# Kernel optimization log

Hardware: AMD Instinct MI355X
Metric: run time of the kernel (lower is better)

## Reference

```python
import jax, jax.numpy as jnp
import numpy as np

B, N, E0, F_IN, H, EMB, VEC, DPI = 1024, 256, 2048, 6, 32, 32, 26, 512


def setup_inputs() -> dict:
    key = jax.random.key(0)
    ks = jax.random.split(key, 16)
    # fixed urban scene graph, shared by every batch element, with self-loops
    src0 = jax.random.randint(ks[0], (E0,), 0, N, dtype=jnp.int32)
    dst0 = jax.random.randint(ks[1], (E0,), 0, N, dtype=jnp.int32)
    loops = jnp.arange(N, dtype=jnp.int32)
    src = jnp.concatenate([src0, loops])
    dst = jnp.concatenate([dst0, loops])

    s = 0.05
    return {
        "graph_feats": jax.random.normal(ks[2], (B, N, F_IN), jnp.float32),
        "vector": jax.random.normal(ks[3], (B, VEC), jnp.float32),
        "src": src,
        "dst": dst,
        "W1": jax.random.normal(ks[4], (F_IN, H), jnp.float32) * s,
        "b1": jnp.zeros((H,), jnp.float32),
        "W2": jax.random.normal(ks[5], (H, H), jnp.float32) * s,
        "b2": jnp.zeros((H,), jnp.float32),
        "W3": jax.random.normal(ks[6], (H, H), jnp.float32) * s,
        "b3": jnp.zeros((H,), jnp.float32),
        "W_emb": jax.random.normal(ks[7], (H, EMB), jnp.float32) * s,
        "b_emb": jnp.zeros((EMB,), jnp.float32),
        "W_pi": jax.random.normal(ks[8], (VEC + EMB, DPI), jnp.float32) * s,
        "b_pi": jnp.zeros((DPI,), jnp.float32),
        "W_vf": jax.random.normal(ks[9], (VEC + EMB, DPI), jnp.float32) * s,
        "b_vf": jnp.zeros((DPI,), jnp.float32),
    }


def _edge_norm(src, dst, n_nodes):
    # DGL GraphConv norm='both': out_deg(src)^-1/2 * in_deg(dst)^-1/2
    ones = jnp.ones(src.shape[0], jnp.float32)
    deg_out = jax.ops.segment_sum(ones, src, num_segments=n_nodes)
    deg_in = jax.ops.segment_sum(ones, dst, num_segments=n_nodes)
    inv_o = jnp.where(deg_out > 0, deg_out ** -0.5, 0.0)
    inv_i = jnp.where(deg_in > 0, deg_in ** -0.5, 0.0)
    return inv_o[src] * inv_i[dst]  # [E]


def _gconv(h, src, dst, norm, W, b):
    # h: [B, N, F]; symmetric-normalized aggregation then linear (DGL GraphConv)
    msg = h[:, src, :] * norm[None, :, None]          # [B, E, F]
    agg = jnp.zeros_like(h).at[:, dst, :].add(msg)     # [B, N, F]
    return agg @ W + b


def reference(graph_feats, vector, src, dst, W1, b1, W2, b2, W3, b3,
              W_emb, b_emb, W_pi, b_pi, W_vf, b_vf):
    n_nodes = graph_feats.shape[1]
    norm = _edge_norm(src, dst, n_nodes)
    h = jax.nn.relu(_gconv(graph_feats, src, dst, norm, W1, b1))
    h = jax.nn.relu(_gconv(h, src, dst, norm, W2, b2))
    h = jax.nn.relu(_gconv(h, src, dst, norm, W3, b3))  # three_layers=True
    hg = jnp.mean(h, axis=1)                 # dgl.mean_nodes -> [B, H]
    emb = hg @ W_emb + b_emb                 # [B, EMB]
    comb = jnp.concatenate([vector[:, :26], emb], axis=1)  # [B, 58]
    pi = jax.nn.relu(comb @ W_pi + b_pi)
    vf = jax.nn.relu(comb @ W_vf + b_vf)
    return pi, vf
```

## Files before the change

### kernel.cpp

```cpp
#include <hip/hip_runtime.h>
#include <hip/hip_fp16.h>

#define B_    1024
#define N_    256
#define E_    2304
#define EPT_  9
#define FIN_  6
#define VEC_  26
#define HSTR_ 40
#define BPB_  2

typedef _Float16 half8 __attribute__((ext_vector_type(8)));
typedef float    f32x4 __attribute__((ext_vector_type(4)));

__global__ __launch_bounds__(512) void fused_kernel(
    const float* __restrict__ gf,
    const float* __restrict__ vec,
    const int* __restrict__ src, const int* __restrict__ dst,
    const float* __restrict__ W1, const float* __restrict__ b1,
    const float* __restrict__ W2, const float* __restrict__ b2,
    const float* __restrict__ W3, const float* __restrict__ b3,
    const float* __restrict__ We, const float* __restrict__ be,
    const float* __restrict__ Wpi, const float* __restrict__ bpi,
    const float* __restrict__ Wvf, const float* __restrict__ bvf,
    float2* __restrict__ out)
{
    __shared__ __align__(16) __half hbuf[BPB_][N_ * HSTR_];
    __shared__ unsigned int packedE[E_];
    __shared__ float part[BPB_][8 * 33];
    __shared__ float hgl[BPB_][32];
    __shared__ float combS[BPB_][64];
    __shared__ int   wsum[4];

    const int t  = threadIdx.x;
    const int u  = t & 255;
    const int bh = t >> 8;
    const int b0 = blockIdx.x * BPB_;
    const int lane = t & 63, wv = t >> 6;

    int*   deg_o  = (int*)&hbuf[0][0];
    int*   deg_i  = (int*)&hbuf[0][0] + 256;
    int*   scanA  = (int*)&hbuf[0][0] + 512;
    int*   cursor = (int*)&hbuf[0][0] + 768;
    int*   perm   = (int*)&hbuf[0][0] + 1024;
    float* inv_o  = (float*)&hbuf[0][0] + 1280;
    float* inv_i  = (float*)&hbuf[0][0] + 1536;
    int*   bcnt   = (int*)&hbuf[0][0] + 1792;
    int*   boff   = (int*)&hbuf[0][0] + 1856;

    if (t < 256) {
        deg_o[t] = 0; deg_i[t] = 0;
        if (t < 64) bcnt[t] = 0;
    }
    __syncthreads();

    int sB[EPT_], dB[EPT_];
    if (t < 256) {
#pragma unroll
        for (int i = 0; i < EPT_; ++i) { int e = t + 256 * i; sB[i] = src[e]; dB[i] = dst[e]; }
#pragma unroll
        for (int i = 0; i < EPT_; ++i) { atomicAdd(&deg_o[sB[i]], 1); atomicAdd(&deg_i[dB[i]], 1); }
    }
    __syncthreads();

    int x = 0, dI = 0, bucket = 0;
    if (t < 256) {
        dI = deg_i[t];
        {
            int dO = deg_o[t];
            inv_o[t] = dO > 0 ? rsqrtf((float)dO) : 0.f;
            inv_i[t] = dI > 0 ? rsqrtf((float)dI) : 0.f;
        }
        x = dI;
#pragma unroll
        for (int d = 1; d < 64; d <<= 1) {
            int y = __shfl_up(x, d, 64);
            if (lane >= d) x += y;
        }
        if (lane == 63) wsum[wv] = x;
        bucket = dI > 63 ? 63 : dI;
        atomicAdd(&bcnt[bucket], 1);
    }
    __syncthreads();

    if (t < 256) {
        int prefix = 0;
#pragma unroll
        for (int w = 0; w < 3; ++w) if (w < wv) prefix += wsum[w];
        int incl = x + prefix;
        scanA[t]  = incl;
        cursor[t] = incl - dI;
    }
    if (t < 64) {
        int c = bcnt[t], xx = c;
#pragma unroll
        for (int d = 1; d < 64; d <<= 1) {
            int y = __shfl_up(xx, d, 64);
            if (lane >= d) xx += y;
        }
        boff[t] = xx - c;
    }
    __syncthreads();

    if (t < 256) {
        { int pos = atomicAdd(&boff[bucket], 1); perm[pos] = t; }
#pragma unroll
        for (int i = 0; i < EPT_; ++i) {
            int s = sB[i], dd = dB[i];
            int pos = atomicAdd(&cursor[dd], 1);
            float nrm = inv_o[s] * inv_i[dd];
            unsigned short hh = __half_as_ushort(__float2half(nrm));
            packedE[pos] = ((unsigned int)s << 16) | (unsigned int)hh;
        }
    }
    __syncthreads();

    const int node = perm[u];
    const int end  = scanA[node];
    const int beg  = end - deg_i[node];
    __syncthreads();

    {
        const float* g = gf + (size_t)(b0 + bh) * (N_ * FIN_);
        for (int i = u; i < N_ * 8; i += 256) {
            int n = i >> 3, k = i & 7;
            hbuf[bh][n * HSTR_ + k] = __float2half((k < FIN_) ? g[n * FIN_ + k] : 0.f);
        }
    }
    __syncthreads();

    const __half2 z2 = __float2half2_rn(0.f);

    {
        __half2 a2[4] = {z2, z2, z2, z2};
        for (int e = beg; e < end; ++e) {
            unsigned int uu = packedE[e];
            __half2 w2 = __half2half2(__ushort_as_half((unsigned short)(uu & 0xffffu)));
            int ro = (uu >> 16) * HSTR_;
            union { float4 f4; __half2 h2[4]; } r;
            r.f4 = *(const float4*)&hbuf[bh][ro];
#pragma unroll
            for (int q = 0; q < 4; ++q) a2[q] = __hfma2(w2, r.h2[q], a2[q]);
        }
        float o[32];
#pragma unroll
        for (int j = 0; j < 32; ++j) o[j] = b1[j];
#pragma unroll
        for (int k = 0; k < FIN_; ++k) {
            float ak = (k & 1) ? __high2float(a2[k >> 1]) : __low2float(a2[k >> 1]);
            const float* wr = &W1[k * 32];
#pragma unroll
            for (int j = 0; j < 32; ++j) o[j] += ak * wr[j];
        }
        __syncthreads();
        union { float4 f4; __half2 h2[4]; } w;
        float4* row = (float4*)&hbuf[bh][node * HSTR_];
#pragma unroll
        for (int q = 0; q < 4; ++q) {
#pragma unroll
            for (int r = 0; r < 4; ++r)
                w.h2[r] = __floats2half2_rn(fmaxf(o[8*q + 2*r], 0.f), fmaxf(o[8*q + 2*r + 1], 0.f));
            row[q] = w.f4;
        }
    }
    __syncthreads();

    const int m16  = lane & 15;
    const int q4   = lane >> 4;
    const int slab = (wv & 3) * 64;
    const int wb   = wv >> 2;

    for (int L = 0; L < 2; ++L) {
        const float* Wl = (L == 0) ? W2 : W3;
        const float* Bl = (L == 0) ? b2 : b3;

        half8 bfrag[2];
        float bias_c[2];
#pragma unroll
        for (int cb = 0; cb < 2; ++cb) {
            int col = m16 + 16 * cb;
#pragma unroll
            for (int j = 0; j < 8; ++j)
                bfrag[cb][j] = (_Float16)Wl[(q4 * 8 + j) * 32 + col];
            bias_c[cb] = Bl[col];
        }

        __half2 acc2[16];
#pragma unroll
        for (int j = 0; j < 16; ++j) acc2[j] = z2;
        for (int e = beg; e < end; ++e) {
            unsigned int uu = packedE[e];
            __half2 w2 = __half2half2(__ushort_as_half((unsigned short)(uu & 0xffffu)));
            int ro = (uu >> 16) * HSTR_;
            const float4* hr = (const float4*)&hbuf[bh][ro];
            union { float4 f4; __half2 h2[4]; } r0, r1, r2, r3;
            r0.f4 = hr[0]; r1.f4 = hr[1]; r2.f4 = hr[2]; r3.f4 = hr[3];
#pragma unroll
            for (int q = 0; q < 4; ++q) {
                acc2[q]      = __hfma2(w2, r0.h2[q], acc2[q]);
                acc2[4 + q]  = __hfma2(w2, r1.h2[q], acc2[4 + q]);
                acc2[8 + q]  = __hfma2(w2, r2.h2[q], acc2[8 + q]);
                acc2[12 + q] = __hfma2(w2, r3.h2[q], acc2[12 + q]);
            }
        }
        __syncthreads();
        {
            union { float4 f4; __half2 h2[4]; } w;
            float4* row = (float4*)&hbuf[bh][node * HSTR_];
#pragma unroll
            for (int q = 0; q < 4; ++q) {
#pragma unroll
                for (int r = 0; r < 4; ++r) w.h2[r] = acc2[4 * q + r];
                row[q] = w.f4;
            }
        }
        __syncthreads();

        {
            half8 afrag[4];
#pragma unroll
            for (int g = 0; g < 4; ++g) {
                union { float4 f4; half8 h8; } uf;
                uf.f4 = *(const float4*)&hbuf[wb][(slab + g * 16 + m16) * HSTR_ + q4 * 8];
                afrag[g] = uf.h8;
            }
            f32x4 D[4][2];
#pragma unroll
            for (int g = 0; g < 4; ++g) {
#pragma unroll
                for (int cb = 0; cb < 2; ++cb) {
                    f32x4 c = {bias_c[cb], bias_c[cb], bias_c[cb], bias_c[cb]};
                    D[g][cb] = __builtin_amdgcn_mfma_f32_16x16x32_f16(afrag[g], bfrag[cb], c, 0, 0, 0);
                }
            }
#pragma unroll
            for (int g = 0; g < 4; ++g) {
#pragma unroll
                for (int cb = 0; cb < 2; ++cb) {
#pragma unroll
                    for (int r = 0; r < 4; ++r) {
                        float v = fmaxf(D[g][cb][r], 0.f);
                        hbuf[wb][(slab + g * 16 + q4 * 4 + r) * HSTR_ + cb * 16 + m16] = __float2half(v);
                    }
                }
            }
        }
        __syncthreads();
    }

    {
        int j = u & 31, g8 = u >> 5;
        float s = 0.f;
        for (int i = 0; i < 32; ++i)
            s += __half2float(hbuf[bh][(g8 * 32 + i) * HSTR_ + j]);
        part[bh][g8 * 33 + j] = s;
    }
    __syncthreads();
    if (t < 64) {
        int bb = t >> 5, j = t & 31;
        float sum = 0.f;
#pragma unroll
        for (int g8 = 0; g8 < 8; ++g8) sum += part[bb][g8 * 33 + j];
        hgl[bb][j] = sum * (1.0f / 256.0f);
    }
    if (t < BPB_ * VEC_) {
        int bb = t / VEC_, j = t - bb * VEC_;
        combS[bb][j] = vec[(b0 + bb) * VEC_ + j];
    }
    __syncthreads();

    if (t < 64) {
        int bb = t >> 5, j = t & 31;
        float v = be[j];
#pragma unroll
        for (int k = 0; k < 32; ++k) v += hgl[bb][k] * We[k * 32 + j];
        combS[bb][VEC_ + j] = v;
    }
    __syncthreads();

    {
        const float* Wm = (bh == 0) ? Wpi : Wvf;
        const float* bm = (bh == 0) ? bpi : bvf;
        const float2 bp = ((const float2*)bm)[u];
        float2 a0 = bp, a1 = bp;
        const float2* Wr = (const float2*)Wm;
        for (int k = 0; k < VEC_ + 32; ++k) {
            float2 a = Wr[k * 256 + u];
            float c0 = combS[0][k];
            float c1 = combS[1][k];
            a0.x += c0 * a.x; a0.y += c0 * a.y;
            a1.x += c1 * a.x; a1.y += c1 * a.y;
        }
        int base = bh * 262144;
        out[base + b0 * 256 + u]       = make_float2(fmaxf(a0.x, 0.f), fmaxf(a0.y, 0.f));
        out[base + (b0 + 1) * 256 + u] = make_float2(fmaxf(a1.x, 0.f), fmaxf(a1.y, 0.f));
    }
}

extern "C" void kernel_launch(void* const* d_in, const int* in_sizes, int n_in,
                              void* d_out, int out_size, void* d_ws, size_t ws_size,
                              hipStream_t stream)
{
    fused_kernel<<<B_ / BPB_, 512, 0, stream>>>(
        (const float*)d_in[0], (const float*)d_in[1],
        (const int*)d_in[2], (const int*)d_in[3],
        (const float*)d_in[4], (const float*)d_in[5],
        (const float*)d_in[6], (const float*)d_in[7],
        (const float*)d_in[8], (const float*)d_in[9],
        (const float*)d_in[10], (const float*)d_in[11],
        (const float*)d_in[12], (const float*)d_in[13],
        (const float*)d_in[14], (const float*)d_in[15],
        (float2*)d_out);
}
```

Baseline: 114.0 us.

## Split feature columns across two thread halves with 1024-thread blocks

Doubles the block size so each node's aggregation in layers 2-3 is split across two threads, each handling 16 of the 32 features. The MFMA output columns are likewise split across wave groups. This roughly halves per-thread registers and serial work in the gather loop, exposing more parallelism. In exchange, edge metadata is read twice, layer 1 and the tail leave half the threads idle, and an extra barrier is added.

```diff
diff --git a/kernel.cpp b/kernel.cpp
--- a/kernel.cpp
+++ b/kernel.cpp
@@ -13,7 +13,7 @@
 typedef _Float16 half8 __attribute__((ext_vector_type(8)));
 typedef float    f32x4 __attribute__((ext_vector_type(4)));
 
-__global__ __launch_bounds__(512) void fused_kernel(
+__global__ __launch_bounds__(1024) void fused_kernel(
     const float* __restrict__ gf,
     const float* __restrict__ vec,
     const int* __restrict__ src, const int* __restrict__ dst,
@@ -34,7 +34,8 @@
 
     const int t  = threadIdx.x;
     const int u  = t & 255;
-    const int bh = t >> 8;
+    const int bh = (t >> 8) & 1;
+    const int eh = t >> 9;
     const int b0 = blockIdx.x * BPB_;
     const int lane = t & 63, wv = t >> 6;
 
@@ -122,7 +123,7 @@
 
     {
         const float* g = gf + (size_t)(b0 + bh) * (N_ * FIN_);
-        for (int i = u; i < N_ * 8; i += 256) {
+        for (int i = u + 256 * eh; i < N_ * 8; i += 512) {
             int n = i >> 3, k = i & 7;
             hbuf[bh][n * HSTR_ + k] = __float2half((k < FIN_) ? g[n * FIN_ + k] : 0.f);
         }
@@ -132,75 +133,77 @@
     const __half2 z2 = __float2half2_rn(0.f);
 
     {
-        __half2 a2[4] = {z2, z2, z2, z2};
-        for (int e = beg; e < end; ++e) {
-            unsigned int uu = packedE[e];
-            __half2 w2 = __half2half2(__ushort_as_half((unsigned short)(uu & 0xffffu)));
-            int ro = (uu >> 16) * HSTR_;
-            union { float4 f4; __half2 h2[4]; } r;
-            r.f4 = *(const float4*)&hbuf[bh][ro];
-#pragma unroll
-            for (int q = 0; q < 4; ++q) a2[q] = __hfma2(w2, r.h2[q], a2[q]);
-        }
         float o[32];
-#pragma unroll
-        for (int j = 0; j < 32; ++j) o[j] = b1[j];
-#pragma unroll
-        for (int k = 0; k < FIN_; ++k) {
-            float ak = (k & 1) ? __high2float(a2[k >> 1]) : __low2float(a2[k >> 1]);
-            const float* wr = &W1[k * 32];
-#pragma unroll
-            for (int j = 0; j < 32; ++j) o[j] += ak * wr[j];
+        if (eh == 0) {
+            __half2 a2[4] = {z2, z2, z2, z2};
+            for (int e = beg; e < end; ++e) {
+                unsigned int uu = packedE[e];
+                __half2 w2 = __half2half2(__ushort_as_half((unsigned short)(uu & 0xffffu)));
+                int ro = (uu >> 16) * HSTR_;
+                union { float4 f4; __half2 h2[4]; } r;
+                r.f4 = *(const float4*)&hbuf[bh][ro];
+#pragma unroll
+                for (int q = 0; q < 4; ++q) a2[q] = __hfma2(w2, r.h2[q], a2[q]);
+            }
+#pragma unroll
+            for (int j = 0; j < 32; ++j) o[j] = b1[j];
+#pragma unroll
+            for (int k = 0; k < FIN_; ++k) {
+                float ak = (k & 1) ? __high2float(a2[k >> 1]) : __low2float(a2[k >> 1]);
+                const float* wr = &W1[k * 32];
+#pragma unroll
+                for (int j = 0; j < 32; ++j) o[j] += ak * wr[j];
+            }
         }
         __syncthreads();
-        union { float4 f4; __half2 h2[4]; } w;
-        float4* row = (float4*)&hbuf[bh][node * HSTR_];
-#pragma unroll
-        for (int q = 0; q < 4; ++q) {
-#pragma unroll
-            for (int r = 0; r < 4; ++r)
-                w.h2[r] = __floats2half2_rn(fmaxf(o[8*q + 2*r], 0.f), fmaxf(o[8*q + 2*r + 1], 0.f));
-            row[q] = w.f4;
+        if (eh == 0) {
+            union { float4 f4; __half2 h2[4]; } w;
+            float4* row = (float4*)&hbuf[bh][node * HSTR_];
+#pragma unroll
+            for (int q = 0; q < 4; ++q) {
+#pragma unroll
+                for (int r = 0; r < 4; ++r)
+                    w.h2[r] = __floats2half2_rn(fmaxf(o[8*q + 2*r], 0.f), fmaxf(o[8*q + 2*r + 1], 0.f));
+                row[q] = w.f4;
+            }
         }
     }
     __syncthreads();
 
     const int m16  = lane & 15;
     const int q4   = lane >> 4;
+    const int wb   = (wv >> 2) & 1;
+    const int wch  = wv >> 3;
     const int slab = (wv & 3) * 64;
-    const int wb   = wv >> 2;
 
     for (int L = 0; L < 2; ++L) {
         const float* Wl = (L == 0) ? W2 : W3;
         const float* Bl = (L == 0) ? b2 : b3;
 
-        half8 bfrag[2];
-        float bias_c[2];
-#pragma unroll
-        for (int cb = 0; cb < 2; ++cb) {
-            int col = m16 + 16 * cb;
+        half8 bfrag;
+        float bias_c;
+        {
+            int col = m16 + 16 * wch;
 #pragma unroll
             for (int j = 0; j < 8; ++j)
-                bfrag[cb][j] = (_Float16)Wl[(q4 * 8 + j) * 32 + col];
-            bias_c[cb] = Bl[col];
-        }
-
-        __half2 acc2[16];
-#pragma unroll
-        for (int j = 0; j < 16; ++j) acc2[j] = z2;
+                bfrag[j] = (_Float16)Wl[(q4 * 8 + j) * 32 + col];
+            bias_c = Bl[col];
+        }
+
+        __half2 acc2[8];
+#pragma unroll
+        for (int j = 0; j < 8; ++j) acc2[j] = z2;
         for (int e = beg; e < end; ++e) {
             unsigned int uu = packedE[e];
             __half2 w2 = __half2half2(__ushort_as_half((unsigned short)(uu & 0xffffu)));
             int ro = (uu >> 16) * HSTR_;
             const float4* hr = (const float4*)&hbuf[bh][ro];
-            union { float4 f4; __half2 h2[4]; } r0, r1, r2, r3;
-            r0.f4 = hr[0]; r1.f4 = hr[1]; r2.f4 = hr[2]; r3.f4 = hr[3];
+            union { float4 f4; __half2 h2[4]; } ra, rb;
+            ra.f4 = hr[2 * eh]; rb.f4 = hr[2 * eh + 1];
 #pragma unroll
             for (int q = 0; q < 4; ++q) {
-                acc2[q]      = __hfma2(w2, r0.h2[q], acc2[q]);
-                acc2[4 + q]  = __hfma2(w2, r1.h2[q], acc2[4 + q]);
-                acc2[8 + q]  = __hfma2(w2, r2.h2[q], acc2[8 + q]);
-                acc2[12 + q] = __hfma2(w2, r3.h2[q], acc2[12 + q]);
+                acc2[q]     = __hfma2(w2, ra.h2[q], acc2[q]);
+                acc2[4 + q] = __hfma2(w2, rb.h2[q], acc2[4 + q]);
             }
         }
         __syncthreads();
@@ -208,11 +211,11 @@
             union { float4 f4; __half2 h2[4]; } w;
             float4* row = (float4*)&hbuf[bh][node * HSTR_];
 #pragma unroll
-            for (int q = 0; q < 4; ++q) {
-#pragma unroll
-                for (int r = 0; r < 4; ++r) w.h2[r] = acc2[4 * q + r];
-                row[q] = w.f4;
-            }
+            for (int r = 0; r < 4; ++r) w.h2[r] = acc2[r];
+            row[2 * eh] = w.f4;
+#pragma unroll
+            for (int r = 0; r < 4; ++r) w.h2[r] = acc2[4 + r];
+            row[2 * eh + 1] = w.f4;
         }
         __syncthreads();
 
@@ -224,31 +227,26 @@
                 uf.f4 = *(const float4*)&hbuf[wb][(slab + g * 16 + m16) * HSTR_ + q4 * 8];
                 afrag[g] = uf.h8;
             }
-            f32x4 D[4][2];
+            f32x4 D[4];
 #pragma unroll
             for (int g = 0; g < 4; ++g) {
-#pragma unroll
-                for (int cb = 0; cb < 2; ++cb) {
-                    f32x4 c = {bias_c[cb], bias_c[cb], bias_c[cb], bias_c[cb]};
-                    D[g][cb] = __builtin_amdgcn_mfma_f32_16x16x32_f16(afrag[g], bfrag[cb], c, 0, 0, 0);
+                f32x4 c = {bias_c, bias_c, bias_c, bias_c};
+                D[g] = __builtin_amdgcn_mfma_f32_16x16x32_f16(afrag[g], bfrag, c, 0, 0, 0);
+            }
+            __syncthreads();
+#pragma unroll
+            for (int g = 0; g < 4; ++g) {
+#pragma unroll
+                for (int r = 0; r < 4; ++r) {
+                    float v = fmaxf(D[g][r], 0.f);
+                    hbuf[wb][(slab + g * 16 + q4 * 4 + r) * HSTR_ + wch * 16 + m16] = __float2half(v);
                 }
             }
-#pragma unroll
-            for (int g = 0; g < 4; ++g) {
-#pragma unroll
-                for (int cb = 0; cb < 2; ++cb) {
-#pragma unroll
-                    for (int r = 0; r < 4; ++r) {
-                        float v = fmaxf(D[g][cb][r], 0.f);
-                        hbuf[wb][(slab + g * 16 + q4 * 4 + r) * HSTR_ + cb * 16 + m16] = __float2half(v);
-                    }
-                }
-            }
         }
         __syncthreads();
     }
 
-    {
+    if (t < 512) {
         int j = u & 31, g8 = u >> 5;
         float s = 0.f;
         for (int i = 0; i < 32; ++i)
@@ -278,9 +276,10 @@
     }
     __syncthreads();
 
-    {
-        const float* Wm = (bh == 0) ? Wpi : Wvf;
-        const float* bm = (bh == 0) ? bpi : bvf;
+    if (t < 512) {
+        const int mh = t >> 8;
+        const float* Wm = (mh == 0) ? Wpi : Wvf;
+        const float* bm = (mh == 0) ? bpi : bvf;
         const float2 bp = ((const float2*)bm)[u];
         float2 a0 = bp, a1 = bp;
         const float2* Wr = (const float2*)Wm;
@@ -291,7 +290,7 @@
             a0.x += c0 * a.x; a0.y += c0 * a.y;
             a1.x += c1 * a.x; a1.y += c1 * a.y;
         }
-        int base = bh * 262144;
+        int base = mh * 262144;
         out[base + b0 * 256 + u]       = make_float2(fmaxf(a0.x, 0.f), fmaxf(a0.y, 0.f));
         out[base + (b0 + 1) * 256 + u] = make_float2(fmaxf(a1.x, 0.f), fmaxf(a1.y, 0.f));
     }
@@ -301,7 +300,7 @@
                               void* d_out, int out_size, void* d_ws, size_t ws_size,
                               hipStream_t stream)
 {
-    fused_kernel<<<B_ / BPB_, 512, 0, stream>>>(
+    fused_kernel<<<B_ / BPB_, 1024, 0, stream>>>(
         (const float*)d_in[0], (const float*)d_in[1],
         (const int*)d_in[2], (const int*)d_in[3],
         (const float*)d_in[4], (const float*)d_in[5],
```

New measurement: 125.7 us. +10.3%, slower.
